# Kernel tuning notes

Measured on AMD Instinct MI355X. Metric: run time of the kernel, lower is better.

## Reference

```python
import jax, jax.numpy as jnp
import numpy as np

N, D, H, E, K = 16384, 1024, 4096, 8, 2
CAPACITY_FACTOR = 1.0
WORLD_SIZE = 1


def setup_inputs() -> dict:
    key = jax.random.key(0)
    ks = jax.random.split(key, 7)
    s = 0.02
    return {
        "x":  jax.random.normal(ks[0], (N, D), dtype=jnp.float32),
        "Wr": jax.random.normal(ks[1], (D, E), dtype=jnp.float32) * s,
        "br": jnp.zeros((E,), dtype=jnp.float32),
        "W1": jax.random.normal(ks[2], (E, D, H), dtype=jnp.float32) * s,
        "b1": jnp.zeros((E, H), dtype=jnp.float32),
        "W2": jax.random.normal(ks[3], (E, H, D), dtype=jnp.float32) * s,
        "b2": jnp.zeros((E, D), dtype=jnp.float32),
    }


def reference(x, Wr, br, W1, b1, W2, b2):
    n_tok = x.shape[0]
    capacity = max(int(CAPACITY_FACTOR * n_tok / (K * WORLD_SIZE)), 1)  # static

    # Router (dropout is identity in eval mode)
    logits = x @ Wr + br                      # [N, E]
    probs = jax.nn.softmax(logits, axis=-1)   # [N, E]
    ew, ei = jax.lax.top_k(probs, K)          # [N, K] each

    # Per-token / per-expert assignment mask and routing weight
    match = ei[:, :, None] == jnp.arange(E)[None, None, :]     # [N, K, E]
    mask = match.any(axis=1)                                   # [N, E] bool
    w = (ew[:, :, None] * match).sum(axis=1)                   # [N, E]

    # Capacity: keep first `capacity` tokens per expert in token order
    pos = jnp.cumsum(mask.astype(jnp.int32), axis=0) - 1       # [N, E]
    keep = mask & (pos < capacity)                             # [N, E]
    keepT = keep.T                                             # [E, N]

    # Gather kept token ids per expert (stable sort keeps token order);
    # padding slots have valid=False and contribute zeros.
    sel = jax.vmap(lambda k: jnp.argsort(jnp.logical_not(k))[:capacity])(keepT)  # [E, C]
    valid = jnp.take_along_axis(keepT, sel, axis=1)            # [E, C]

    # Dispatch + per-expert MLP (Expert: Linear -> ReLU -> Linear)
    xg = x[sel]                                                # [E, C, D]
    h = jax.nn.relu(jnp.einsum('ecd,edh->ech', xg, W1) + b1[:, None, :])
    out = jnp.einsum('ech,ehd->ecd', h, W2) + b2[:, None, :]   # [E, C, D]

    wg = jax.vmap(lambda s, wc: wc[s])(sel, w.T)               # [E, C]
    weighted = out * (wg * valid.astype(out.dtype))[..., None]

    # Scatter-add combine
    final = jnp.zeros_like(x).at[sel.reshape(-1)].add(weighted.reshape(-1, x.shape[-1]))

    # Aux losses (world_size = 1)
    expert_counts = mask.astype(probs.dtype).sum(axis=0)       # [E]
    density = probs.mean(axis=0)
    usage = expert_counts / n_tok
    balance_loss = (density * usage).sum() * E
    importance = probs.sum(axis=0)
    importance_loss = (importance ** 2).mean()
    aux_loss = balance_loss + importance_loss

    return final, aux_loss
```

## Files before the change

### kernel.cpp

```cpp
#include <hip/hip_runtime.h>
#include <stdint.h>

#define N_TOK 16384
#define DIM   1024
#define HID   4096
#define NE    8
#define CAP   8192
#define MAXSLOT 33792
#define BM 128
#define BN 128
#define BK 32

typedef __attribute__((ext_vector_type(8))) __bf16 bf16x8;
typedef __attribute__((ext_vector_type(4))) float  f32x4;

__device__ inline unsigned short f2bf(float f) {
  unsigned u = __builtin_bit_cast(unsigned, f);
  u += 0x7fffu + ((u >> 16) & 1u);
  return (unsigned short)(u >> 16);
}

__device__ inline void gload_lds16(const void* g, void* l) {
  __builtin_amdgcn_global_load_lds((__attribute__((address_space(1))) void*)(g),
                                   (__attribute__((address_space(3))) void*)(l),
                                   16, 0, 0);
}

__global__ __launch_bounds__(256) void router_kernel(
    const float* __restrict__ x, const float* __restrict__ Wr, const float* __restrict__ br,
    int2* __restrict__ tokE, float2* __restrict__ tokW,
    float* __restrict__ probs_sum, int* __restrict__ mask_count)
{
  __shared__ float s_ps[NE];
  __shared__ int   s_mc[NE];
  int tid = threadIdx.x;
  if (tid < NE) { s_ps[tid] = 0.f; s_mc[tid] = 0; }
  __syncthreads();
  int wave = tid >> 6, lane = tid & 63;
  for (int i = 0; i < 2; ++i) {
    int token = blockIdx.x * 8 + wave * 2 + i;
    float acc[NE];
#pragma unroll
    for (int e = 0; e < NE; ++e) acc[e] = 0.f;
    const float* xr = x + (size_t)token * DIM;
#pragma unroll
    for (int j = 0; j < 4; ++j) {
      int d0 = j * 256 + lane * 4;
      float4 xv = *(const float4*)(xr + d0);
#pragma unroll
      for (int q = 0; q < 4; ++q) {
        float xs = (&xv.x)[q];
        const float* wr = Wr + (size_t)(d0 + q) * NE;
#pragma unroll
        for (int e = 0; e < NE; ++e) acc[e] += xs * wr[e];
      }
    }
#pragma unroll
    for (int ofs = 32; ofs >= 1; ofs >>= 1)
#pragma unroll
      for (int e = 0; e < NE; ++e) acc[e] += __shfl_xor(acc[e], ofs, 64);
    float m = -1e30f;
#pragma unroll
    for (int e = 0; e < NE; ++e) { acc[e] += br[e]; m = fmaxf(m, acc[e]); }
    float s = 0.f;
#pragma unroll
    for (int e = 0; e < NE; ++e) { acc[e] = __expf(acc[e] - m); s += acc[e]; }
    float inv = 1.f / s;
#pragma unroll
    for (int e = 0; e < NE; ++e) acc[e] *= inv;
    int e0 = 0; float p0 = acc[0];
#pragma unroll
    for (int e = 1; e < NE; ++e) if (acc[e] > p0) { p0 = acc[e]; e0 = e; }
    int e1 = -1; float p1 = -1.f;
#pragma unroll
    for (int e = 0; e < NE; ++e) if (e != e0 && acc[e] > p1) { p1 = acc[e]; e1 = e; }
    if (lane == 0) {
      tokE[token] = make_int2(e0, e1);
      tokW[token] = make_float2(p0, p1);
#pragma unroll
      for (int e = 0; e < NE; ++e) atomicAdd(&s_ps[e], acc[e]);
      atomicAdd(&s_mc[e0], 1); atomicAdd(&s_mc[e1], 1);
    }
  }
  __syncthreads();
  if (tid < NE) { atomicAdd(&probs_sum[tid], s_ps[tid]); atomicAdd(&mask_count[tid], s_mc[tid]); }
}

__global__ __launch_bounds__(512) void scan_kernel(
    const int2* __restrict__ tokE, const float2* __restrict__ tokW,
    const int* __restrict__ mask_count,
    int* __restrict__ offPad, int* __restrict__ slotTok, float* __restrict__ slotW)
{
  int wave = threadIdx.x >> 6, lane = threadIdx.x & 63;
  int eid = wave;
  int offs[NE + 1]; offs[0] = 0;
  int off = 0;
  for (int e = 0; e < NE; ++e) {
    int kept = min(mask_count[e], CAP);
    if (e == eid) off = offs[e];
    offs[e + 1] = offs[e] + ((kept + 127) & ~127);
  }
  if (wave == 0 && lane <= NE) offPad[lane] = offs[lane];
  int running = 0;
  for (int base = 0; base < N_TOK; base += 64) {
    int t = base + lane;
    int2 e2 = tokE[t]; float2 w2 = tokW[t];
    bool match = (e2.x == eid) || (e2.y == eid);
    float wgt = (e2.x == eid) ? w2.x : w2.y;
    unsigned long long bal = __ballot(match);
    int pre = __popcll(bal & ((1ull << lane) - 1ull));
    if (match) {
      int pos = running + pre;
      if (pos < CAP) { slotTok[off + pos] = t; slotW[off + pos] = wgt; }
    }
    running += __popcll(bal);
  }
  int kept = min(running, CAP);
  int padded = (kept + 127) & ~127;
  for (int i = kept + lane; i < padded; i += 64) { slotTok[off + i] = 0; slotW[off + i] = 0.f; }
}

__global__ void aux_kernel(const float* __restrict__ probs_sum,
                           const int* __restrict__ mask_count, float* __restrict__ out_aux)
{
  if (threadIdx.x == 0 && blockIdx.x == 0) {
    float bal = 0.f, imp = 0.f;
    for (int e = 0; e < NE; ++e) {
      float ps = probs_sum[e];
      bal += (ps / N_TOK) * ((float)mask_count[e] / N_TOK);
      imp += ps * ps;
    }
    out_aux[0] = bal * NE + imp / NE;
  }
}

__global__ __launch_bounds__(256) void gather_kernel(
    const float* __restrict__ x, const int* __restrict__ slotTok,
    const int* __restrict__ offPad, unsigned short* __restrict__ Xg)
{
  int total = offPad[NE];
  int wave = threadIdx.x >> 6, lane = threadIdx.x & 63;
  int slot = blockIdx.x * 4 + wave;
  if (slot >= total) return;
  int token = slotTok[slot];
  const float* src = x + (size_t)token * DIM;
  unsigned short* dst = Xg + (size_t)slot * DIM;
#pragma unroll
  for (int j = 0; j < 4; ++j) {
    int idx = j * 256 + lane * 4;
    float4 v = *(const float4*)(src + idx);
    ushort4 o;
    o.x = f2bf(v.x); o.y = f2bf(v.y); o.z = f2bf(v.z); o.w = f2bf(v.w);
    *(ushort4*)(dst + idx) = o;
  }
}

__global__ __launch_bounds__(256) void transpose_cvt(
    const float* __restrict__ src, unsigned short* __restrict__ dst, int R, int C)
{
  __shared__ float tile[64][65];
  int e = blockIdx.z;
  int cb = blockIdx.x * 64, rb = blockIdx.y * 64;
  int tid = threadIdx.x;
  int tr = tid >> 6, tc = tid & 63;
  const float* s = src + (size_t)e * R * C;
  unsigned short* d = dst + (size_t)e * R * C;
#pragma unroll
  for (int it = 0; it < 16; ++it) {
    int r = it * 4 + tr;
    tile[r][tc] = s[(size_t)(rb + r) * C + cb + tc];
  }
  __syncthreads();
#pragma unroll
  for (int it = 0; it < 16; ++it) {
    int r = it * 4 + tr;
    d[(size_t)(cb + r) * R + rb + tc] = f2bf(tile[tc][r]);
  }
}

__global__ __launch_bounds__(256) void gemm1_kernel(
    const unsigned short* __restrict__ Xg, const unsigned short* __restrict__ W1t,
    const float* __restrict__ b1, const int* __restrict__ offPad,
    unsigned short* __restrict__ Hbuf, int eBase, int compactH)
{
  int e = eBase + blockIdx.z;
  int off = offPad[e];
  int mtiles = (offPad[e + 1] - off) >> 7;
  if ((int)blockIdx.y >= mtiles) return;
  int row0 = off + blockIdx.y * BM;
  int col0 = blockIdx.x * BN;
  int hrow0 = compactH ? row0 : (int)(blockIdx.y * BM);

  __shared__ alignas(16) unsigned short As[BM * BK];
  __shared__ alignas(16) unsigned short Bs[BN * BK];

  int tid = threadIdx.x;
  int wave = tid >> 6, lane = tid & 63;
  const unsigned short* Aptr = Xg + (size_t)row0 * DIM;
  const unsigned short* Bptr = W1t + (size_t)e * HID * DIM + (size_t)col0 * DIM;
  int ldRow = tid >> 2, ldCol = (tid & 3) * 8;

  f32x4 acc[4][4];
#pragma unroll
  for (int i = 0; i < 4; ++i)
#pragma unroll
    for (int j = 0; j < 4; ++j) acc[i][j] = f32x4{0.f, 0.f, 0.f, 0.f};

  int wm = (wave & 1) * 64, wn = (wave >> 1) * 64;
  int quad = lane >> 4, r16 = lane & 15;
  unsigned short* AsW = As + wave * 512;
  unsigned short* BsW = Bs + wave * 512;

  for (int kb = 0; kb < DIM; kb += BK) {
#pragma unroll
    for (int r = 0; r < 2; ++r) {
      gload_lds16(Aptr + (size_t)(r * 64 + ldRow) * DIM + kb + ldCol, AsW + r * 2048);
      gload_lds16(Bptr + (size_t)(r * 64 + ldRow) * DIM + kb + ldCol, BsW + r * 2048);
    }
    asm volatile("s_waitcnt vmcnt(0)" ::: "memory");
    __syncthreads();
    bf16x8 af[4], bfr[4];
#pragma unroll
    for (int i = 0; i < 4; ++i) af[i]  = *reinterpret_cast<const bf16x8*>(&As[(wm + i * 16 + r16) * BK + quad * 8]);
#pragma unroll
    for (int j = 0; j < 4; ++j) bfr[j] = *reinterpret_cast<const bf16x8*>(&Bs[(wn + j * 16 + r16) * BK + quad * 8]);
#pragma unroll
    for (int i = 0; i < 4; ++i)
#pragma unroll
      for (int j = 0; j < 4; ++j)
        acc[i][j] = __builtin_amdgcn_mfma_f32_16x16x32_bf16(af[i], bfr[j], acc[i][j], 0, 0, 0);
    __syncthreads();
  }
#pragma unroll
  for (int j = 0; j < 4; ++j) {
    int gc = col0 + wn + j * 16 + r16;
    float bias = b1[(size_t)e * HID + gc];
#pragma unroll
    for (int i = 0; i < 4; ++i)
#pragma unroll
      for (int r = 0; r < 4; ++r) {
        int lr = wm + i * 16 + quad * 4 + r;
        float v = fmaxf(acc[i][j][r] + bias, 0.f);
        Hbuf[(size_t)(hrow0 + lr) * HID + gc] = f2bf(v);
      }
  }
}

__global__ __launch_bounds__(256) void gemm2_kernel(
    const unsigned short* __restrict__ Hbuf, const unsigned short* __restrict__ W2t,
    const float* __restrict__ b2, const int* __restrict__ offPad,
    const int* __restrict__ slotTok, const float* __restrict__ slotW,
    float* __restrict__ outF, int eBase, int compactH)
{
  int e = eBase + blockIdx.z;
  int off = offPad[e];
  int mtiles = (offPad[e + 1] - off) >> 7;
  if ((int)blockIdx.y >= mtiles) return;
  int row0 = off + blockIdx.y * BM;
  int col0 = blockIdx.x * BN;
  int hrow0 = compactH ? row0 : (int)(blockIdx.y * BM);

  __shared__ alignas(16) unsigned short As[BM * BK];
  __shared__ alignas(16) unsigned short Bs[BN * BK];
  __shared__ int   sTok[BM];
  __shared__ float sW[BM];

  int tid = threadIdx.x;
  int wave = tid >> 6, lane = tid & 63;
  const unsigned short* Aptr = Hbuf + (size_t)hrow0 * HID;
  const unsigned short* Bptr = W2t + (size_t)e * DIM * HID + (size_t)col0 * HID;
  int ldRow = tid >> 2, ldCol = (tid & 3) * 8;

  f32x4 acc[4][4];
#pragma unroll
  for (int i = 0; i < 4; ++i)
#pragma unroll
    for (int j = 0; j < 4; ++j) acc[i][j] = f32x4{0.f, 0.f, 0.f, 0.f};

  int wm = (wave & 1) * 64, wn = (wave >> 1) * 64;
  int quad = lane >> 4, r16 = lane & 15;
  unsigned short* AsW = As + wave * 512;
  unsigned short* BsW = Bs + wave * 512;

  for (int kb = 0; kb < HID; kb += BK) {
#pragma unroll
    for (int r = 0; r < 2; ++r) {
      gload_lds16(Aptr + (size_t)(r * 64 + ldRow) * HID + kb + ldCol, AsW + r * 2048);
      gload_lds16(Bptr + (size_t)(r * 64 + ldRow) * HID + kb + ldCol, BsW + r * 2048);
    }
    asm volatile("s_waitcnt vmcnt(0)" ::: "memory");
    __syncthreads();
    bf16x8 af[4], bfr[4];
#pragma unroll
    for (int i = 0; i < 4; ++i) af[i]  = *reinterpret_cast<const bf16x8*>(&As[(wm + i * 16 + r16) * BK + quad * 8]);
#pragma unroll
    for (int j = 0; j < 4; ++j) bfr[j] = *reinterpret_cast<const bf16x8*>(&Bs[(wn + j * 16 + r16) * BK + quad * 8]);
#pragma unroll
    for (int i = 0; i < 4; ++i)
#pragma unroll
      for (int j = 0; j < 4; ++j)
        acc[i][j] = __builtin_amdgcn_mfma_f32_16x16x32_bf16(af[i], bfr[j], acc[i][j], 0, 0, 0);
    __syncthreads();
  }
  if (tid < BM) { sTok[tid] = slotTok[row0 + tid]; sW[tid] = slotW[row0 + tid]; }
  __syncthreads();
#pragma unroll
  for (int j = 0; j < 4; ++j) {
    int gc = col0 + wn + j * 16 + r16;
    float bias = b2[(size_t)e * DIM + gc];
#pragma unroll
    for (int i = 0; i < 4; ++i)
#pragma unroll
      for (int r = 0; r < 4; ++r) {
        int lr = wm + i * 16 + quad * 4 + r;
        float v = (acc[i][j][r] + bias) * sW[lr];
        atomicAdd(&outF[(size_t)sTok[lr] * DIM + gc], v);
      }
  }
}

extern "C" void kernel_launch(void* const* d_in, const int* in_sizes, int n_in,
                              void* d_out, int out_size, void* d_ws, size_t ws_size,
                              hipStream_t stream)
{
  const float* x  = (const float*)d_in[0];
  const float* Wr = (const float*)d_in[1];
  const float* br = (const float*)d_in[2];
  const float* W1 = (const float*)d_in[3];
  const float* b1 = (const float*)d_in[4];
  const float* W2 = (const float*)d_in[5];
  const float* b2 = (const float*)d_in[6];
  float* outF = (float*)d_out;

  char* ws = (char*)d_ws;
  size_t off = 0;
  auto alloc = [&](size_t bytes) -> char* {
    char* p = ws + off; off += (bytes + 255) & ~(size_t)255; return p;
  };
  char* meta = alloc(4096);
  float* probs_sum = (float*)meta;
  int*   mask_count = (int*)(meta + 64);
  int*   offPad = (int*)(meta + 128);
  int2*  tokE = (int2*)alloc((size_t)N_TOK * 8);
  float2* tokW = (float2*)alloc((size_t)N_TOK * 8);
  int*   slotTok = (int*)alloc((size_t)MAXSLOT * 4);
  float* slotW = (float*)alloc((size_t)MAXSLOT * 4);
  unsigned short* Xg  = (unsigned short*)alloc((size_t)MAXSLOT * DIM * 2);
  unsigned short* W1t = (unsigned short*)alloc((size_t)NE * HID * DIM * 2);
  unsigned short* W2t = (unsigned short*)alloc((size_t)NE * DIM * HID * 2);
  size_t hFull = (size_t)MAXSLOT * HID * 2;
  size_t hOne  = (size_t)CAP * HID * 2;
  bool compact = (off + hFull) <= ws_size;
  unsigned short* Hbuf = (unsigned short*)alloc(compact ? hFull : hOne);

  hipMemsetAsync(meta, 0, 4096, stream);
  hipMemsetAsync(d_out, 0, (size_t)out_size * 4, stream);

  transpose_cvt<<<dim3(HID / 64, DIM / 64, NE), 256, 0, stream>>>(W1, W1t, DIM, HID);
  transpose_cvt<<<dim3(DIM / 64, HID / 64, NE), 256, 0, stream>>>(W2, W2t, HID, DIM);
  router_kernel<<<dim3(N_TOK / 8), 256, 0, stream>>>(x, Wr, br, tokE, tokW, probs_sum, mask_count);
  scan_kernel<<<dim3(1), 512, 0, stream>>>(tokE, tokW, mask_count, offPad, slotTok, slotW);
  aux_kernel<<<dim3(1), 64, 0, stream>>>(probs_sum, mask_count, outF + (size_t)N_TOK * DIM);
  gather_kernel<<<dim3(MAXSLOT / 4), 256, 0, stream>>>(x, slotTok, offPad, Xg);

  if (compact) {
    gemm1_kernel<<<dim3(HID / BN, CAP / BM, NE), 256, 0, stream>>>(Xg, W1t, b1, offPad, Hbuf, 0, 1);
    gemm2_kernel<<<dim3(DIM / BN, CAP / BM, NE), 256, 0, stream>>>(Hbuf, W2t, b2, offPad, slotTok, slotW, outF, 0, 1);
  } else {
    for (int e = 0; e < NE; ++e) {
      gemm1_kernel<<<dim3(HID / BN, CAP / BM, 1), 256, 0, stream>>>(Xg, W1t, b1, offPad, Hbuf, e, 0);
      gemm2_kernel<<<dim3(DIM / BN, CAP / BM, 1), 256, 0, stream>>>(Hbuf, W2t, b2, offPad, slotTok, slotW, outF, e, 0);
    }
  }
}
```

Before: 1.535 ms.

## Double-buffer LDS in expert GEMMs, remap tiles across XCDs, batch scan loads

Both expert GEMM kernels now use two LDS buffers, issuing the next K-slice's global-to-LDS loads right after the barrier so they overlap the MFMA work, and the trailing barrier per iteration is dropped. Block indices are remapped so consecutive blocks landing on the same XCD share M-tiles, aiming at better L2 reuse of A/B tiles. The scan kernel loads eight 64-token chunks at once to raise memory-level parallelism. The cost is doubled LDS per block, which may lower occupancy. The remap assumes the grid block count is a multiple of 8, and the earlier sTok/sW load now relies on the loop barriers for visibility.

```diff
diff --git a/kernel.cpp b/kernel.cpp
--- a/kernel.cpp
+++ b/kernel.cpp
@@ -26,6 +26,14 @@
                                    16, 0, 0);
 }
 
+__device__ inline void xcd_remap(int& mtile, int& ntile) {
+  int f = blockIdx.y * gridDim.x + blockIdx.x;
+  int c = f & 7, q = f >> 3;
+  int nT = gridDim.x;
+  ntile = q % nT;
+  mtile = (q / nT) * 8 + c;
+}
+
 __global__ __launch_bounds__(256) void router_kernel(
     const float* __restrict__ x, const float* __restrict__ Wr, const float* __restrict__ br,
     int2* __restrict__ tokE, float2* __restrict__ tokW,
@@ -102,18 +110,26 @@
   }
   if (wave == 0 && lane <= NE) offPad[lane] = offs[lane];
   int running = 0;
-  for (int base = 0; base < N_TOK; base += 64) {
-    int t = base + lane;
-    int2 e2 = tokE[t]; float2 w2 = tokW[t];
-    bool match = (e2.x == eid) || (e2.y == eid);
-    float wgt = (e2.x == eid) ? w2.x : w2.y;
-    unsigned long long bal = __ballot(match);
-    int pre = __popcll(bal & ((1ull << lane) - 1ull));
-    if (match) {
-      int pos = running + pre;
-      if (pos < CAP) { slotTok[off + pos] = t; slotW[off + pos] = wgt; }
-    }
-    running += __popcll(bal);
+  for (int base = 0; base < N_TOK; base += 512) {
+    int2 e2a[8]; float2 w2a[8];
+#pragma unroll
+    for (int u = 0; u < 8; ++u) {
+      int t = base + u * 64 + lane;
+      e2a[u] = tokE[t]; w2a[u] = tokW[t];
+    }
+#pragma unroll
+    for (int u = 0; u < 8; ++u) {
+      int t = base + u * 64 + lane;
+      bool match = (e2a[u].x == eid) || (e2a[u].y == eid);
+      float wgt = (e2a[u].x == eid) ? w2a[u].x : w2a[u].y;
+      unsigned long long bal = __ballot(match);
+      int pre = __popcll(bal & ((1ull << lane) - 1ull));
+      if (match) {
+        int pos = running + pre;
+        if (pos < CAP) { slotTok[off + pos] = t; slotW[off + pos] = wgt; }
+      }
+      running += __popcll(bal);
+    }
   }
   int kept = min(running, CAP);
   int padded = (kept + 127) & ~127;
@@ -186,13 +202,15 @@
   int e = eBase + blockIdx.z;
   int off = offPad[e];
   int mtiles = (offPad[e + 1] - off) >> 7;
-  if ((int)blockIdx.y >= mtiles) return;
-  int row0 = off + blockIdx.y * BM;
-  int col0 = blockIdx.x * BN;
-  int hrow0 = compactH ? row0 : (int)(blockIdx.y * BM);
-
-  __shared__ alignas(16) unsigned short As[BM * BK];
-  __shared__ alignas(16) unsigned short Bs[BN * BK];
+  int mtile, ntile;
+  xcd_remap(mtile, ntile);
+  if (mtile >= mtiles) return;
+  int row0 = off + mtile * BM;
+  int col0 = ntile * BN;
+  int hrow0 = compactH ? row0 : mtile * BM;
+
+  __shared__ alignas(16) unsigned short As[2][BM * BK];
+  __shared__ alignas(16) unsigned short Bs[2][BN * BK];
 
   int tid = threadIdx.x;
   int wave = tid >> 6, lane = tid & 63;
@@ -208,28 +226,31 @@
 
   int wm = (wave & 1) * 64, wn = (wave >> 1) * 64;
   int quad = lane >> 4, r16 = lane & 15;
-  unsigned short* AsW = As + wave * 512;
-  unsigned short* BsW = Bs + wave * 512;
-
+
+  auto stage = [&](int buf, int kb) {
+#pragma unroll
+    for (int r = 0; r < 2; ++r) {
+      gload_lds16(Aptr + (size_t)(r * 64 + ldRow) * DIM + kb + ldCol, &As[buf][wave * 512 + r * 2048]);
+      gload_lds16(Bptr + (size_t)(r * 64 + ldRow) * DIM + kb + ldCol, &Bs[buf][wave * 512 + r * 2048]);
+    }
+  };
+
+  stage(0, 0);
   for (int kb = 0; kb < DIM; kb += BK) {
-#pragma unroll
-    for (int r = 0; r < 2; ++r) {
-      gload_lds16(Aptr + (size_t)(r * 64 + ldRow) * DIM + kb + ldCol, AsW + r * 2048);
-      gload_lds16(Bptr + (size_t)(r * 64 + ldRow) * DIM + kb + ldCol, BsW + r * 2048);
-    }
+    int cur = (kb >> 5) & 1;
     asm volatile("s_waitcnt vmcnt(0)" ::: "memory");
     __syncthreads();
+    if (kb + BK < DIM) stage(cur ^ 1, kb + BK);
     bf16x8 af[4], bfr[4];
 #pragma unroll
-    for (int i = 0; i < 4; ++i) af[i]  = *reinterpret_cast<const bf16x8*>(&As[(wm + i * 16 + r16) * BK + quad * 8]);
-#pragma unroll
-    for (int j = 0; j < 4; ++j) bfr[j] = *reinterpret_cast<const bf16x8*>(&Bs[(wn + j * 16 + r16) * BK + quad * 8]);
+    for (int i = 0; i < 4; ++i) af[i]  = *reinterpret_cast<const bf16x8*>(&As[cur][(wm + i * 16 + r16) * BK + quad * 8]);
+#pragma unroll
+    for (int j = 0; j < 4; ++j) bfr[j] = *reinterpret_cast<const bf16x8*>(&Bs[cur][(wn + j * 16 + r16) * BK + quad * 8]);
 #pragma unroll
     for (int i = 0; i < 4; ++i)
 #pragma unroll
       for (int j = 0; j < 4; ++j)
         acc[i][j] = __builtin_amdgcn_mfma_f32_16x16x32_bf16(af[i], bfr[j], acc[i][j], 0, 0, 0);
-    __syncthreads();
   }
 #pragma unroll
   for (int j = 0; j < 4; ++j) {
@@ -255,13 +276,15 @@
   int e = eBase + blockIdx.z;
   int off = offPad[e];
   int mtiles = (offPad[e + 1] - off) >> 7;
-  if ((int)blockIdx.y >= mtiles) return;
-  int row0 = off + blockIdx.y * BM;
-  int col0 = blockIdx.x * BN;
-  int hrow0 = compactH ? row0 : (int)(blockIdx.y * BM);
-
-  __shared__ alignas(16) unsigned short As[BM * BK];
-  __shared__ alignas(16) unsigned short Bs[BN * BK];
+  int mtile, ntile;
+  xcd_remap(mtile, ntile);
+  if (mtile >= mtiles) return;
+  int row0 = off + mtile * BM;
+  int col0 = ntile * BN;
+  int hrow0 = compactH ? row0 : mtile * BM;
+
+  __shared__ alignas(16) unsigned short As[2][BM * BK];
+  __shared__ alignas(16) unsigned short Bs[2][BN * BK];
   __shared__ int   sTok[BM];
   __shared__ float sW[BM];
 
@@ -279,31 +302,34 @@
 
   int wm = (wave & 1) * 64, wn = (wave >> 1) * 64;
   int quad = lane >> 4, r16 = lane & 15;
-  unsigned short* AsW = As + wave * 512;
-  unsigned short* BsW = Bs + wave * 512;
-
+
+  auto stage = [&](int buf, int kb) {
+#pragma unroll
+    for (int r = 0; r < 2; ++r) {
+      gload_lds16(Aptr + (size_t)(r * 64 + ldRow) * HID + kb + ldCol, &As[buf][wave * 512 + r * 2048]);
+      gload_lds16(Bptr + (size_t)(r * 64 + ldRow) * HID + kb + ldCol, &Bs[buf][wave * 512 + r * 2048]);
+    }
+  };
+
+  if (tid < BM) { sTok[tid] = slotTok[row0 + tid]; sW[tid] = slotW[row0 + tid]; }
+
+  stage(0, 0);
   for (int kb = 0; kb < HID; kb += BK) {
-#pragma unroll
-    for (int r = 0; r < 2; ++r) {
-      gload_lds16(Aptr + (size_t)(r * 64 + ldRow) * HID + kb + ldCol, AsW + r * 2048);
-      gload_lds16(Bptr + (size_t)(r * 64 + ldRow) * HID + kb + ldCol, BsW + r * 2048);
-    }
+    int cur = (kb >> 5) & 1;
     asm volatile("s_waitcnt vmcnt(0)" ::: "memory");
     __syncthreads();
+    if (kb + BK < HID) stage(cur ^ 1, kb + BK);
     bf16x8 af[4], bfr[4];
 #pragma unroll
-    for (int i = 0; i < 4; ++i) af[i]  = *reinterpret_cast<const bf16x8*>(&As[(wm + i * 16 + r16) * BK + quad * 8]);
-#pragma unroll
-    for (int j = 0; j < 4; ++j) bfr[j] = *reinterpret_cast<const bf16x8*>(&Bs[(wn + j * 16 + r16) * BK + quad * 8]);
+    for (int i = 0; i < 4; ++i) af[i]  = *reinterpret_cast<const bf16x8*>(&As[cur][(wm + i * 16 + r16) * BK + quad * 8]);
+#pragma unroll
+    for (int j = 0; j < 4; ++j) bfr[j] = *reinterpret_cast<const bf16x8*>(&Bs[cur][(wn + j * 16 + r16) * BK + quad * 8]);
 #pragma unroll
     for (int i = 0; i < 4; ++i)
 #pragma unroll
       for (int j = 0; j < 4; ++j)
         acc[i][j] = __builtin_amdgcn_mfma_f32_16x16x32_bf16(af[i], bfr[j], acc[i][j], 0, 0, 0);
-    __syncthreads();
-  }
-  if (tid < BM) { sTok[tid] = slotTok[row0 + tid]; sW[tid] = slotW[row0 + tid]; }
-  __syncthreads();
+  }
 #pragma unroll
   for (int j = 0; j < 4; ++j) {
     int gc = col0 + wn + j * 16 + r16;
```

Measured after the change: 1.602 ms. 4.4% more time.
